# Kernel optimization log

Measured on AMD Instinct MI355X. Metric: run time of the kernel, lower is better.

## Reference

```python
import jax, jax.numpy as jnp
import numpy as np

NUM_LAYERS = 4
D_MODEL = 1024
N_HEAD = 16
D_FF = 1024
BATCH = 2
LONG = 2048
SHORT = 256


def setup_inputs() -> dict:
    key = jax.random.key(0)
    ks = jax.random.split(key, 6)
    s = 0.02
    L, D, F = NUM_LAYERS, D_MODEL, D_FF
    S = LONG + SHORT
    return {
        "x": jax.random.normal(ks[0], (BATCH, S, D), jnp.float32),
        "Wqkv": jax.random.normal(ks[1], (L, 3 * D, D), jnp.float32) * s,
        "bqkv": jnp.zeros((L, 3 * D), jnp.float32),
        "Wo": jax.random.normal(ks[2], (L, D, D), jnp.float32) * s,
        "bo": jnp.zeros((L, D), jnp.float32),
        "W1": jax.random.normal(ks[3], (L, F, D), jnp.float32) * s,
        "b1": jnp.zeros((L, F), jnp.float32),
        "W2": jax.random.normal(ks[4], (L, D, F), jnp.float32) * s,
        "b2": jnp.zeros((L, D), jnp.float32),
        "ln1_w": jnp.ones((L, D), jnp.float32),
        "ln1_b": jnp.zeros((L, D), jnp.float32),
        "ln2_w": jnp.ones((L, D), jnp.float32),
        "ln2_b": jnp.zeros((L, D), jnp.float32),
        "norm_w": jnp.ones((D,), jnp.float32),
        "norm_b": jnp.zeros((D,), jnp.float32),
        "long_seq_length": LONG,
        "num_short_seqs": SHORT,
    }


def _ln(x, w, b, eps=1e-5):
    m = jnp.mean(x, axis=-1, keepdims=True)
    v = jnp.mean(jnp.square(x - m), axis=-1, keepdims=True)
    return (x - m) * jax.lax.rsqrt(v + eps) * w + b


def _build_mask(long_seq_length, num_short_seqs, dtype):
    S = long_seq_length + num_short_seqs
    # long rows: attend only to long cols; short rows: long cols + own diag
    allowed = jnp.zeros((S, S), bool).at[:, :long_seq_length].set(True)
    sidx = jnp.arange(long_seq_length, S)
    allowed = allowed.at[sidx, sidx].set(True)
    return jnp.where(allowed, jnp.zeros((), dtype), -jnp.inf).astype(dtype)


def reference(x, Wqkv, bqkv, Wo, bo, W1, b1, W2, b2,
              ln1_w, ln1_b, ln2_w, ln2_b, norm_w, norm_b,
              long_seq_length, num_short_seqs):
    # dropout layers are treated as identity (eval / deterministic)
    B, S, D = x.shape
    H = N_HEAD
    dh = D // H
    scale = 1.0 / np.sqrt(dh)
    mask = _build_mask(long_seq_length, num_short_seqs, x.dtype)  # [S,S]

    for l in range(Wqkv.shape[0]):
        # --- nn.TransformerEncoderLayer (post-norm) ---
        qkv = jnp.einsum('bsd,ed->bse', x, Wqkv[l]) + bqkv[l]  # [B,S,3D]
        q, k, v = jnp.split(qkv, 3, axis=-1)
        q = q.reshape(B, S, H, dh).transpose(0, 2, 1, 3)
        k = k.reshape(B, S, H, dh).transpose(0, 2, 1, 3)
        v = v.reshape(B, S, H, dh).transpose(0, 2, 1, 3)
        scores = jnp.einsum('bhsd,bhtd->bhst', q, k) * scale + mask
        attn = jax.nn.softmax(scores, axis=-1)
        ctx = jnp.einsum('bhst,bhtd->bhsd', attn, v)
        ctx = ctx.transpose(0, 2, 1, 3).reshape(B, S, D)
        attn_out = jnp.einsum('bsd,ed->bse', ctx, Wo[l]) + bo[l]
        h = _ln(x + attn_out, ln1_w[l], ln1_b[l])
        ff = jnp.einsum('bsf,df->bsd',
                        jax.nn.relu(jnp.einsum('bsd,fd->bsf', h, W1[l]) + b1[l]),
                        W2[l]) + b2[l]
        y = _ln(h + ff, ln2_w[l], ln2_b[l])
        # --- outer residual + shared LayerNorm ---
        x = _ln(x + y, norm_w, norm_b)
    return x
```

## Files before the change

### kernel.cpp

```cpp
#include <hip/hip_runtime.h>

#define DEV __device__ __forceinline__

typedef short bf16x8 __attribute__((ext_vector_type(8)));
typedef short bf16x4_t __attribute__((ext_vector_type(4)));
typedef float f32x4 __attribute__((ext_vector_type(4)));

#define S_TOT 2304
#define D3    3072
#define NLONG 2048
#define OSTRIDE 4718592L

DEV unsigned short f2b(float f) {
    union { float f; unsigned u; } v; v.f = f;
    unsigned r = v.u + 0x7fffu + ((v.u >> 16) & 1u);
    return (unsigned short)(r >> 16);
}
DEV float b2f(unsigned short u) {
    union { unsigned u; float f; } v; v.u = ((unsigned)u) << 16;
    return v.f;
}

#define GLL16(g, l) __builtin_amdgcn_global_load_lds( \
    (const __attribute__((address_space(1))) void*)(g), \
    (__attribute__((address_space(3))) void*)(l), 16, 0, 0)

DEV bf16x4_t tr_read(unsigned byteaddr) {
    bf16x4_t r;
    asm volatile("ds_read_b64_tr_b16 %0, %1" : "=v"(r) : "v"(byteaddr));
    return r;
}

__global__ __launch_bounds__(256) void k_cast(const float* __restrict__ in,
                                              unsigned short* __restrict__ out, long n) {
    long i = ((long)blockIdx.x * 256 + threadIdx.x) * 4;
    long stride = (long)gridDim.x * 1024;
    for (; i < n; i += stride) {
        float4 v = *(const float4*)(in + i);
        *(ushort4*)(out + i) = make_ushort4(f2b(v.x), f2b(v.y), f2b(v.z), f2b(v.w));
    }
}

__global__ __launch_bounds__(256) void k_castcopy(const float* __restrict__ in,
                                                  float* __restrict__ outf,
                                                  unsigned short* __restrict__ outb, long n) {
    long i = ((long)blockIdx.x * 256 + threadIdx.x) * 4;
    long stride = (long)gridDim.x * 1024;
    for (; i < n; i += stride) {
        float4 v = *(const float4*)(in + i);
        *(float4*)(outf + i) = v;
        *(ushort4*)(outb + i) = make_ushort4(f2b(v.x), f2b(v.y), f2b(v.z), f2b(v.w));
    }
}

template<int BN, int OBF, int RELU>
__global__ __launch_bounds__(256, BN == 128 ? 3 : 4)
void k_gemm(const unsigned short* __restrict__ A,
            const unsigned short* __restrict__ B,
            const float* __restrict__ bias,
            float* __restrict__ Cf,
            unsigned short* __restrict__ Cb,
            int M, int N, int K) {
    __shared__ unsigned short As[3][128 * 32];
    __shared__ unsigned short Bs[3][BN * 32];
    const int tid  = threadIdx.x;
    const int lane = tid & 63;
    const int wave = tid >> 6;
    const int g = lane >> 4, li = lane & 15;

    const int nbm = gridDim.x;
    const int nwg = nbm * gridDim.y;
    int id = blockIdx.x + blockIdx.y * nbm;
    if ((nwg & 7) == 0) id = (id & 7) * (nwg >> 3) + (id >> 3);
    const int bm = id % nbm, bn = id / nbm;

    constexpr int WN = BN / 2;
    constexpr int NF = WN / 16;
    const int wm = (wave >> 1) * 64, wn = (wave & 1) * WN;

    f32x4 acc[4][NF] = {};

    const long abase = (long)bm * 128 * K;
    const long bbase = (long)bn * BN * K;
    const int srow = tid >> 2;
    const int scol = (tid & 3) * 8;

    auto stage = [&](int kt, int buf) {
        GLL16(A + abase + (long)srow * K + kt + scol, As[buf] + tid * 8);
        GLL16(A + abase + (long)(srow + 64) * K + kt + scol, As[buf] + (tid + 256) * 8);
        GLL16(B + bbase + (long)srow * K + kt + scol, Bs[buf] + tid * 8);
        if (BN == 128)
            GLL16(B + bbase + (long)(srow + 64) * K + kt + scol, Bs[buf] + (tid + 256) * 8);
    };

    const int nt = K / 32;
    stage(0, 0);
    stage(32, 1);
    if constexpr (BN == 128) asm volatile("s_waitcnt vmcnt(4)" ::: "memory");
    else                     asm volatile("s_waitcnt vmcnt(3)" ::: "memory");

    for (int t = 0; t < nt; ++t) {
        __builtin_amdgcn_s_barrier();
        __builtin_amdgcn_sched_barrier(0);
        asm volatile("" ::: "memory");
        if (t + 2 < nt) stage((t + 2) * 32, (t + 2) % 3);
        const unsigned short* Ab = As[t % 3];
        const unsigned short* Bb = Bs[t % 3];
        bf16x8 af[4], bfr[NF];
#pragma unroll
        for (int mf = 0; mf < 4; ++mf)
            af[mf] = *(const bf16x8*)(Ab + (wm + mf * 16 + li) * 32 + g * 8);
#pragma unroll
        for (int nf = 0; nf < NF; ++nf)
            bfr[nf] = *(const bf16x8*)(Bb + (wn + nf * 16 + li) * 32 + g * 8);
#pragma unroll
        for (int mf = 0; mf < 4; ++mf)
#pragma unroll
            for (int nf = 0; nf < NF; ++nf)
                acc[mf][nf] = __builtin_amdgcn_mfma_f32_16x16x32_bf16(af[mf], bfr[nf], acc[mf][nf], 0, 0, 0);
        if (t + 2 < nt) {
            if constexpr (BN == 128) asm volatile("s_waitcnt vmcnt(4)" ::: "memory");
            else                     asm volatile("s_waitcnt vmcnt(3)" ::: "memory");
        } else {
            asm volatile("s_waitcnt vmcnt(0)" ::: "memory");
        }
    }

#pragma unroll
    for (int nf = 0; nf < NF; ++nf) {
        int col = bn * BN + wn + nf * 16 + li;
        float bv = bias[col];
#pragma unroll
        for (int mf = 0; mf < 4; ++mf) {
#pragma unroll
            for (int i = 0; i < 4; ++i) {
                int row = bm * 128 + wm + mf * 16 + g * 4 + i;
                float v = acc[mf][nf][i] + bv;
                if (RELU) v = fmaxf(v, 0.f);
                if (OBF) Cb[(long)row * N + col] = f2b(v);
                else     Cf[(long)row * N + col] = v;
            }
        }
    }
}

__global__ __launch_bounds__(256, 3) void k_attn(const unsigned short* __restrict__ qkv,
                                                 float* __restrict__ Opart,
                                                 float* __restrict__ lpart) {
    __shared__ unsigned short Ks[2][4096];
    __shared__ unsigned short Vt[2][4096];
    __shared__ unsigned short Ps[4][2048];

    const int tid  = threadIdx.x;
    const int lane = tid & 63, wave = tid >> 6;
    const int g = lane >> 4, li = lane & 15;
    const int bq = blockIdx.x, h = blockIdx.y;
    const int b = blockIdx.z & 1, chunk = blockIdx.z >> 1;
    const int q0 = bq * 128 + wave * 32;
    const int koff = chunk * 1024;

    const long baseQ = ((long)b * S_TOT) * D3 + h * 64;
    const long baseK = baseQ + 1024;
    const long baseV = baseQ + 2048;

    bf16x8 qf[2][2];
#pragma unroll
    for (int mf = 0; mf < 2; ++mf)
#pragma unroll
        for (int kk = 0; kk < 2; ++kk)
            qf[mf][kk] = *(const bf16x8*)(qkv + baseQ + (long)(q0 + mf * 16 + li) * D3 + kk * 32 + g * 8);

    f32x4 O[2][4] = {};
    float psum[2][4] = {};

    unsigned short* Pw = Ps[wave];
    const unsigned pwb = (unsigned)(size_t)Pw + lane * 8u;

    auto stage = [&](int ti, int buf) {
        const int kt = koff + ti * 64;
#pragma unroll
        for (int r = 0; r < 2; ++r) {
            int s = tid + r * 256;
            int kr = s >> 3, si = s & 7;
            GLL16(qkv + baseK + (long)(kt + kr) * D3 + ((si ^ (kr & 7)) * 8), Ks[buf] + s * 8);
        }
#pragma unroll
        for (int r = 0; r < 2; ++r) {
            int i = tid + r * 256;
            int vt = ((i >> 5) << 2) + ((i & 7) >> 1);
            int vd = (((i >> 3) & 3) << 4) + ((i & 1) << 3);
            GLL16(qkv + baseV + (long)(kt + vt) * D3 + vd, Vt[buf] + i * 8);
        }
    };

    auto compute = [&](int cur) {
        f32x4 sc[2][4] = {};
        const unsigned short* Kb = Ks[cur];
#pragma unroll
        for (int kk = 0; kk < 2; ++kk) {
            bf16x8 kf[4];
#pragma unroll
            for (int nf = 0; nf < 4; ++nf) {
                int kr = nf * 16 + li;
                int slot = (kk * 4 + g) ^ (kr & 7);
                kf[nf] = *(const bf16x8*)(Kb + kr * 64 + slot * 8);
            }
#pragma unroll
            for (int mf = 0; mf < 2; ++mf)
#pragma unroll
                for (int nf = 0; nf < 4; ++nf)
                    sc[mf][nf] = __builtin_amdgcn_mfma_f32_16x16x32_bf16(qf[mf][kk], kf[nf], sc[mf][nf], 0, 0, 0);
        }
#pragma unroll
        for (int mf = 0; mf < 2; ++mf) {
#pragma unroll
            for (int nf = 0; nf < 4; ++nf) {
                float p0 = __expf(sc[mf][nf][0] * 0.125f);
                float p1 = __expf(sc[mf][nf][1] * 0.125f);
                float p2 = __expf(sc[mf][nf][2] * 0.125f);
                float p3 = __expf(sc[mf][nf][3] * 0.125f);
                psum[mf][0] += p0; psum[mf][1] += p1;
                psum[mf][2] += p2; psum[mf][3] += p3;
                unsigned lo, hi;
                asm("v_cvt_pk_bf16_f32 %0, %1, %2" : "=v"(lo) : "v"(p0), "v"(p1));
                asm("v_cvt_pk_bf16_f32 %0, %1, %2" : "=v"(hi) : "v"(p2), "v"(p3));
                unsigned idx = (unsigned)(g * 4 + (li & 3) * 16 + (nf * 2 + (li >> 3)) * 64 +
                                          ((li >> 2) & 1) * 512 + mf * 1024);
                *(uint2*)(Pw + idx) = make_uint2(lo, hi);
            }
        }
        asm volatile("" ::: "memory");
        bf16x4_t pa[2][2][2];
#pragma unroll
        for (int mf = 0; mf < 2; ++mf)
#pragma unroll
            for (int kk = 0; kk < 2; ++kk) {
                unsigned base = pwb + 2u * (unsigned)(kk * 256 + mf * 1024);
                pa[mf][kk][0] = tr_read(base);
                pa[mf][kk][1] = tr_read(base + 1024u);
            }
        const unsigned vtb = (unsigned)(size_t)(&Vt[cur][0]) + lane * 8u + (unsigned)(lane >> 4) * 896u;
        bf16x4_t vr[2][4][2];
#pragma unroll
        for (int kk = 0; kk < 2; ++kk)
#pragma unroll
            for (int nfd = 0; nfd < 4; ++nfd) {
                unsigned base = vtb + (unsigned)(kk * 4096 + nfd * 128);
                vr[kk][nfd][0] = tr_read(base);
                vr[kk][nfd][1] = tr_read(base + 512u);
            }
        asm volatile("s_waitcnt lgkmcnt(0)" ::: "memory");
        __builtin_amdgcn_sched_barrier(0);
#pragma unroll
        for (int kk = 0; kk < 2; ++kk) {
#pragma unroll
            for (int mf = 0; mf < 2; ++mf) {
                bf16x8 paf = __builtin_shufflevector(pa[mf][kk][0], pa[mf][kk][1],
                                                     0, 1, 2, 3, 4, 5, 6, 7);
#pragma unroll
                for (int nfd = 0; nfd < 4; ++nfd) {
                    bf16x8 vf = __builtin_shufflevector(vr[kk][nfd][0], vr[kk][nfd][1],
                                                        0, 1, 2, 3, 4, 5, 6, 7);
                    O[mf][nfd] = __builtin_amdgcn_mfma_f32_16x16x32_bf16(paf, vf, O[mf][nfd], 0, 0, 0);
                }
            }
        }
    };

    stage(0, 0);
    for (int ti = 0; ti < 16; ++ti) {
        __syncthreads();
        if (ti + 1 < 16) stage(ti + 1, (ti + 1) & 1);
        compute(ti & 1);
    }

    float lrow[2][4];
#pragma unroll
    for (int mf = 0; mf < 2; ++mf)
#pragma unroll
        for (int i = 0; i < 4; ++i) {
            float s = psum[mf][i];
#pragma unroll
            for (int off = 1; off < 16; off <<= 1) s += __shfl_xor(s, off);
            lrow[mf][i] = s;
        }

    float* Od = Opart + (long)chunk * OSTRIDE;
    const long bh = ((long)b * 16 + h) * 2304;
#pragma unroll
    for (int mf = 0; mf < 2; ++mf) {
#pragma unroll
        for (int i = 0; i < 4; ++i) {
            int q = q0 + mf * 16 + g * 4 + i;
            long ob = (bh + q) * 64;
#pragma unroll
            for (int nfd = 0; nfd < 4; ++nfd)
                Od[ob + nfd * 16 + li] = O[mf][nfd][i];
            if (li == 0)
                lpart[((long)(chunk * 2 + b) * 16 + h) * 2304 + q] = lrow[mf][i];
        }
    }
}

__global__ __launch_bounds__(256) void k_comb(const unsigned short* __restrict__ qkv,
                                              const float* __restrict__ Opart,
                                              const float* __restrict__ lpart,
                                              unsigned short* __restrict__ ctx) {
    const int q = blockIdx.x % S_TOT;
    const int b = blockIdx.x / S_TOT;
    const int tid = threadIdx.x;
    const int h = tid >> 4;
    const int d0 = (tid & 15) * 4;

    const long idx = (((long)b * 16 + h) * 2304 + q) * 64 + d0;
    float4 O1 = *(const float4*)(Opart + idx);
    float4 O2 = *(const float4*)(Opart + OSTRIDE + idx);
    float den = lpart[((long)b * 16 + h) * 2304 + q] +
                lpart[((long)(2 + b) * 16 + h) * 2304 + q];
    float4 num = make_float4(O1.x + O2.x, O1.y + O2.y, O1.z + O2.z, O1.w + O2.w);

    if (q >= NLONG) {
        const long qb = ((long)b * S_TOT + q) * D3 + h * 64 + d0;
        ushort4 qv = *(const ushort4*)(qkv + qb);
        ushort4 kv = *(const ushort4*)(qkv + qb + 1024);
        float dot = b2f(qv.x) * b2f(kv.x) + b2f(qv.y) * b2f(kv.y) +
                    b2f(qv.z) * b2f(kv.z) + b2f(qv.w) * b2f(kv.w);
#pragma unroll
        for (int off = 1; off < 16; off <<= 1) dot += __shfl_xor(dot, off);
        float pe = __expf(dot * 0.125f);
        ushort4 vv = *(const ushort4*)(qkv + qb + 2048);
        num.x += pe * b2f(vv.x); num.y += pe * b2f(vv.y);
        num.z += pe * b2f(vv.z); num.w += pe * b2f(vv.w);
        den += pe;
    }
    float inv = 1.0f / den;
    long ob = ((long)b * S_TOT + q) * 1024 + h * 64 + d0;
    *(ushort4*)(ctx + ob) = make_ushort4(f2b(num.x * inv), f2b(num.y * inv),
                                         f2b(num.z * inv), f2b(num.w * inv));
}

DEV void block_reduce2(float& sum, float& sq, float* sbuf, int tid) {
#pragma unroll
    for (int off = 32; off > 0; off >>= 1) {
        sum += __shfl_xor(sum, off);
        sq  += __shfl_xor(sq, off);
    }
    __syncthreads();
    if ((tid & 63) == 0) { sbuf[(tid >> 6) * 2] = sum; sbuf[(tid >> 6) * 2 + 1] = sq; }
    __syncthreads();
    sum = sbuf[0] + sbuf[2] + sbuf[4] + sbuf[6];
    sq  = sbuf[1] + sbuf[3] + sbuf[5] + sbuf[7];
}

__global__ __launch_bounds__(256) void k_ln_resid(const float* __restrict__ xa,
                                                  const float* __restrict__ xb,
                                                  const float* __restrict__ w,
                                                  const float* __restrict__ bs,
                                                  float* __restrict__ outf,
                                                  unsigned short* __restrict__ outb) {
    __shared__ float sbuf[8];
    const int tid = threadIdx.x;
    const long base = (long)blockIdx.x * 1024 + tid * 4;
    float4 a = *(const float4*)(xa + base);
    float4 b4 = *(const float4*)(xb + base);
    float4 s = make_float4(a.x + b4.x, a.y + b4.y, a.z + b4.z, a.w + b4.w);
    float sum = s.x + s.y + s.z + s.w;
    float sq = s.x * s.x + s.y * s.y + s.z * s.z + s.w * s.w;
    block_reduce2(sum, sq, sbuf, tid);
    float mean = sum * (1.f / 1024.f);
    float rstd = rsqrtf(sq * (1.f / 1024.f) - mean * mean + 1e-5f);
    float4 wv = *(const float4*)(w + tid * 4);
    float4 bv = *(const float4*)(bs + tid * 4);
    float4 o = make_float4((s.x - mean) * rstd * wv.x + bv.x,
                           (s.y - mean) * rstd * wv.y + bv.y,
                           (s.z - mean) * rstd * wv.z + bv.z,
                           (s.w - mean) * rstd * wv.w + bv.w);
    *(float4*)(outf + base) = o;
    *(ushort4*)(outb + base) = make_ushort4(f2b(o.x), f2b(o.y), f2b(o.z), f2b(o.w));
}

__global__ __launch_bounds__(256) void k_ln_double(const float* __restrict__ h,
                                                   const float* __restrict__ ff,
                                                   const float* __restrict__ x,
                                                   const float* __restrict__ w2,
                                                   const float* __restrict__ bb2,
                                                   const float* __restrict__ nw,
                                                   const float* __restrict__ nb,
                                                   float* __restrict__ outf,
                                                   unsigned short* __restrict__ outb) {
    __shared__ float sbuf[8];
    const int tid = threadIdx.x;
    const long base = (long)blockIdx.x * 1024 + tid * 4;
    float4 hv = *(const float4*)(h + base);
    float4 fv = *(const float4*)(ff + base);
    float4 s = make_float4(hv.x + fv.x, hv.y + fv.y, hv.z + fv.z, hv.w + fv.w);
    float sum = s.x + s.y + s.z + s.w;
    float sq = s.x * s.x + s.y * s.y + s.z * s.z + s.w * s.w;
    block_reduce2(sum, sq, sbuf, tid);
    float mean = sum * (1.f / 1024.f);
    float rstd = rsqrtf(sq * (1.f / 1024.f) - mean * mean + 1e-5f);
    float4 wv = *(const float4*)(w2 + tid * 4);
    float4 bv = *(const float4*)(bb2 + tid * 4);
    float4 y = make_float4((s.x - mean) * rstd * wv.x + bv.x,
                           (s.y - mean) * rstd * wv.y + bv.y,
                           (s.z - mean) * rstd * wv.z + bv.z,
                           (s.w - mean) * rstd * wv.w + bv.w);
    float4 xv = *(const float4*)(x + base);
    float4 t = make_float4(xv.x + y.x, xv.y + y.y, xv.z + y.z, xv.w + y.w);
    sum = t.x + t.y + t.z + t.w;
    sq = t.x * t.x + t.y * t.y + t.z * t.z + t.w * t.w;
    block_reduce2(sum, sq, sbuf, tid);
    mean = sum * (1.f / 1024.f);
    rstd = rsqrtf(sq * (1.f / 1024.f) - mean * mean + 1e-5f);
    float4 nwv = *(const float4*)(nw + tid * 4);
    float4 nbv = *(const float4*)(nb + tid * 4);
    float4 o = make_float4((t.x - mean) * rstd * nwv.x + nbv.x,
                           (t.y - mean) * rstd * nwv.y + nbv.y,
                           (t.z - mean) * rstd * nwv.z + nbv.z,
                           (t.w - mean) * rstd * nwv.w + nbv.w);
    *(float4*)(outf + base) = o;
    *(ushort4*)(outb + base) = make_ushort4(f2b(o.x), f2b(o.y), f2b(o.z), f2b(o.w));
}

extern "C" void kernel_launch(void* const* d_in, const int* in_sizes, int n_in,
                              void* d_out, int out_size, void* d_ws, size_t ws_size,
                              hipStream_t stream) {
    (void)in_sizes; (void)n_in; (void)out_size; (void)ws_size;
    const float* x_in  = (const float*)d_in[0];
    const float* Wqkv  = (const float*)d_in[1];
    const float* bqkv  = (const float*)d_in[2];
    const float* Wo    = (const float*)d_in[3];
    const float* bo    = (const float*)d_in[4];
    const float* W1    = (const float*)d_in[5];
    const float* b1    = (const float*)d_in[6];
    const float* W2    = (const float*)d_in[7];
    const float* b2    = (const float*)d_in[8];
    const float* ln1w  = (const float*)d_in[9];
    const float* ln1b  = (const float*)d_in[10];
    const float* ln2w  = (const float*)d_in[11];
    const float* ln2b  = (const float*)d_in[12];
    const float* nw    = (const float*)d_in[13];
    const float* nb    = (const float*)d_in[14];
    float* xf = (float*)d_out;

    char* p = (char*)d_ws;
    auto alloc = [&](size_t bytes) { char* r = p; p += (bytes + 255) & ~(size_t)255; return r; };
    unsigned short* wqkv_b = (unsigned short*)alloc(12582912UL * 2);
    unsigned short* wo_b   = (unsigned short*)alloc(4194304UL * 2);
    unsigned short* w1_b   = (unsigned short*)alloc(4194304UL * 2);
    unsigned short* w2_b   = (unsigned short*)alloc(4194304UL * 2);
    unsigned short* x_b    = (unsigned short*)alloc(4718592UL * 2);
    unsigned short* qkv_b  = (unsigned short*)alloc(14155776UL * 2);
    unsigned short* ctx_b  = (unsigned short*)alloc(4718592UL * 2);
    unsigned short* h_b    = (unsigned short*)alloc(4718592UL * 2);
    unsigned short* ff1_b  = (unsigned short*)alloc(4718592UL * 2);
    float* of_f  = (float*)alloc(2 * 4718592UL * 4);
    float* h_f   = of_f;
    float* tmp_f = of_f + OSTRIDE;
    float* lpart = (float*)alloc(147456UL * 4);

    k_cast<<<4096, 256, 0, stream>>>(Wqkv, wqkv_b, 12582912L);
    k_cast<<<2048, 256, 0, stream>>>(Wo, wo_b, 4194304L);
    k_cast<<<2048, 256, 0, stream>>>(W1, w1_b, 4194304L);
    k_cast<<<2048, 256, 0, stream>>>(W2, w2_b, 4194304L);
    k_castcopy<<<2048, 256, 0, stream>>>(x_in, xf, x_b, 4718592L);

    for (int l = 0; l < 4; ++l) {
        k_gemm<128, 1, 0><<<dim3(36, 24), 256, 0, stream>>>(x_b, wqkv_b + (size_t)l * 3145728,
                                                            bqkv + l * 3072, nullptr, qkv_b, 4608, 3072, 1024);
        k_attn<<<dim3(18, 16, 4), 256, 0, stream>>>(qkv_b, of_f, lpart);
        k_comb<<<4608, 256, 0, stream>>>(qkv_b, of_f, lpart, ctx_b);
        k_gemm<64, 0, 0><<<dim3(36, 16), 256, 0, stream>>>(ctx_b, wo_b + (size_t)l * 1048576,
                                                           bo + l * 1024, tmp_f, nullptr, 4608, 1024, 1024);
        k_ln_resid<<<4608, 256, 0, stream>>>(xf, tmp_f, ln1w + l * 1024, ln1b + l * 1024, h_f, h_b);
        k_gemm<64, 1, 1><<<dim3(36, 16), 256, 0, stream>>>(h_b, w1_b + (size_t)l * 1048576,
                                                           b1 + l * 1024, nullptr, ff1_b, 4608, 1024, 1024);
        k_gemm<64, 0, 0><<<dim3(36, 16), 256, 0, stream>>>(ff1_b, w2_b + (size_t)l * 1048576,
                                                           b2 + l * 1024, tmp_f, nullptr, 4608, 1024, 1024);
        k_ln_double<<<4608, 256, 0, stream>>>(h_f, tmp_f, xf, ln2w + l * 1024, ln2b + l * 1024,
                                              nw, nb, xf, x_b);
    }
}
```

Measured before the change: 1.121 ms.

## Triple-buffer attention K/V tiles with vmcnt waits, setprio around MFMA, exp2 softmax

Moves the attention kernel's K/V staging from double to triple buffering. Explicit vmcnt waits plus a raw s_barrier replace the per-iteration __syncthreads, so global-to-LDS loads run two tiles ahead of compute. It also raises wave priority around the MFMA blocks and computes exp as a raw v_exp_f32 on pre-scaled scores (scale folded with log2e). The larger LDS footprint drops the occupancy target from 3 to 2 blocks per CU, and the vmcnt counts assume a fixed number of outstanding loads per stage.

```diff
diff --git a/kernel.cpp b/kernel.cpp
--- a/kernel.cpp
+++ b/kernel.cpp
@@ -30,6 +30,12 @@
     asm volatile("ds_read_b64_tr_b16 %0, %1" : "=v"(r) : "v"(byteaddr));
     return r;
 }
+DEV float fexp2(float x) {
+    float r;
+    asm("v_exp_f32 %0, %1" : "=v"(r) : "v"(x));
+    return r;
+}
+#define EXP_SCALE 0.18033688011112042f
 
 __global__ __launch_bounds__(256) void k_cast(const float* __restrict__ in,
                                               unsigned short* __restrict__ out, long n) {
@@ -144,11 +150,11 @@
     }
 }
 
-__global__ __launch_bounds__(256, 3) void k_attn(const unsigned short* __restrict__ qkv,
+__global__ __launch_bounds__(256, 2) void k_attn(const unsigned short* __restrict__ qkv,
                                                  float* __restrict__ Opart,
                                                  float* __restrict__ lpart) {
-    __shared__ unsigned short Ks[2][4096];
-    __shared__ unsigned short Vt[2][4096];
+    __shared__ unsigned short Ks[3][4096];
+    __shared__ unsigned short Vt[3][4096];
     __shared__ unsigned short Ps[4][2048];
 
     const int tid  = threadIdx.x;
@@ -205,20 +211,22 @@
                 int slot = (kk * 4 + g) ^ (kr & 7);
                 kf[nf] = *(const bf16x8*)(Kb + kr * 64 + slot * 8);
             }
+            __builtin_amdgcn_s_setprio(1);
 #pragma unroll
             for (int mf = 0; mf < 2; ++mf)
 #pragma unroll
                 for (int nf = 0; nf < 4; ++nf)
                     sc[mf][nf] = __builtin_amdgcn_mfma_f32_16x16x32_bf16(qf[mf][kk], kf[nf], sc[mf][nf], 0, 0, 0);
+            __builtin_amdgcn_s_setprio(0);
         }
 #pragma unroll
         for (int mf = 0; mf < 2; ++mf) {
 #pragma unroll
             for (int nf = 0; nf < 4; ++nf) {
-                float p0 = __expf(sc[mf][nf][0] * 0.125f);
-                float p1 = __expf(sc[mf][nf][1] * 0.125f);
-                float p2 = __expf(sc[mf][nf][2] * 0.125f);
-                float p3 = __expf(sc[mf][nf][3] * 0.125f);
+                float p0 = fexp2(sc[mf][nf][0] * EXP_SCALE);
+                float p1 = fexp2(sc[mf][nf][1] * EXP_SCALE);
+                float p2 = fexp2(sc[mf][nf][2] * EXP_SCALE);
+                float p3 = fexp2(sc[mf][nf][3] * EXP_SCALE);
                 psum[mf][0] += p0; psum[mf][1] += p1;
                 psum[mf][2] += p2; psum[mf][3] += p3;
                 unsigned lo, hi;
@@ -251,6 +259,7 @@
             }
         asm volatile("s_waitcnt lgkmcnt(0)" ::: "memory");
         __builtin_amdgcn_sched_barrier(0);
+        __builtin_amdgcn_s_setprio(1);
 #pragma unroll
         for (int kk = 0; kk < 2; ++kk) {
 #pragma unroll
@@ -265,13 +274,22 @@
                 }
             }
         }
+        __builtin_amdgcn_s_setprio(0);
     };
 
     stage(0, 0);
+    stage(1, 1);
+    asm volatile("s_waitcnt vmcnt(4)" ::: "memory");
+    asm volatile("s_barrier" ::: "memory");
+    int cur = 0, nb = 2;
     for (int ti = 0; ti < 16; ++ti) {
-        __syncthreads();
-        if (ti + 1 < 16) stage(ti + 1, (ti + 1) & 1);
-        compute(ti & 1);
+        if (ti + 2 < 16) stage(ti + 2, nb);
+        compute(cur);
+        if (ti + 2 < 16)      asm volatile("s_waitcnt vmcnt(4)" ::: "memory");
+        else if (ti == 14)    asm volatile("s_waitcnt vmcnt(0)" ::: "memory");
+        asm volatile("s_barrier" ::: "memory");
+        cur = (cur == 2) ? 0 : cur + 1;
+        nb  = (nb == 2) ? 0 : nb + 1;
     }
 
     float lrow[2][4];
@@ -327,7 +345,7 @@
                     b2f(qv.z) * b2f(kv.z) + b2f(qv.w) * b2f(kv.w);
 #pragma unroll
         for (int off = 1; off < 16; off <<= 1) dot += __shfl_xor(dot, off);
-        float pe = __expf(dot * 0.125f);
+        float pe = fexp2(dot * EXP_SCALE);
         ushort4 vv = *(const ushort4*)(qkv + qb + 2048);
         num.x += pe * b2f(vv.x); num.y += pe * b2f(vv.y);
         num.z += pe * b2f(vv.z); num.w += pe * b2f(vv.w);
```

Result: slower. 1.145 ms (+2.1%).
